# Optimization experiments

Hardware: AMD Instinct MI355X
Metric: run time of the kernel (lower is better)

The kernel has to match this reference:

```python
import jax, jax.numpy as jnp
import numpy as np

D_MODEL = 1024
N_HEADS = 16
D_K = D_MODEL // N_HEADS
SCALE = float(np.sqrt(D_K))


def setup_inputs() -> dict:
    key = jax.random.key(0)
    ks = jax.random.split(key, 9)
    B, L, D = 2, 2048, D_MODEL
    # xavier_uniform with gain 1/sqrt(2): limit = gain*sqrt(6/(fan_in+fan_out))
    limit = (1.0 / np.sqrt(2.0)) * np.sqrt(6.0 / (D + D))
    def xav(k):
        return jax.random.uniform(k, (D, D), jnp.float32, -limit, limit)
    return {
        "query": jax.random.normal(ks[0], (B, L, D), jnp.float32),
        "key": jax.random.normal(ks[1], (B, L, D), jnp.float32),
        "value": jax.random.normal(ks[2], (B, L, D), jnp.float32),
        "mask": jax.random.randint(ks[3], (B, L), 0, 2, jnp.int32),
        "w_q": xav(ks[4]),
        "w_k": xav(ks[5]),
        "w_v": xav(ks[6]),
        "w_o": xav(ks[7]),
        "b_o": jnp.zeros((D,), jnp.float32),
    }


def reference(query, key, value, mask, w_q, w_k, w_v, w_o, b_o):
    B, L, D = query.shape
    H, dk = N_HEADS, D_K
    # torch Linear: x @ W.T ; reshape to (B, H, L, dk)
    def proj(x, w):
        return (x @ w.T).reshape(B, L, H, dk).transpose(0, 2, 1, 3)
    Q = proj(query, w_q)
    K = proj(key, w_k)
    V = proj(value, w_v)
    scores = jnp.einsum("bhqd,bhkd->bhqk", Q, K) / SCALE
    scores = scores.astype(jnp.float32)
    keep = (mask != 0)[:, None, None, :]  # (B,1,1,L)
    scores = jnp.where(keep, scores, jnp.float32(-10000.0))
    attn = jax.nn.softmax(scores, axis=-1).astype(Q.dtype)
    # dropout is identity in eval mode
    ctx = jnp.einsum("bhqk,bhkd->bhqd", attn, V)
    ctx = ctx.transpose(0, 2, 1, 3).reshape(B, L, D)
    return ctx @ w_o.T + b_o
```

## Files before the change

kernel.cpp:

```cpp
#include <hip/hip_runtime.h>

#define DMODEL 1024
#define NHEADS 16
#define BATCH  2
#define SEQ    2048
#define MROWS  (BATCH * SEQ)

typedef unsigned short u16;
typedef unsigned int   u32;
typedef __attribute__((ext_vector_type(8))) short short8v;
typedef __attribute__((ext_vector_type(4))) short short4v;
typedef __attribute__((ext_vector_type(4))) int   int4v;
typedef __attribute__((ext_vector_type(4))) float f32x4;

#define SCALE_LOG2E 0.18033688011112042f

__device__ inline float bf2f(u16 u) {
  union { u32 i; float f; } c; c.i = ((u32)u) << 16; return c.f;
}
__device__ inline u16 f2bf(float f) {
  union { float f; u32 i; } c; c.f = f;
  u32 r = c.i + 0x7fffu + ((c.i >> 16) & 1u);
  return (u16)(r >> 16);
}
__device__ inline short8v ld8(const u16* p) { return *(const short8v*)p; }
__device__ inline short8v cvt8f(const float* p) {
  f32x4 v0 = *(const f32x4*)p;
  f32x4 v1 = *(const f32x4*)(p + 4);
  short8v r;
#pragma unroll
  for (int j = 0; j < 4; ++j) { r[j] = (short)f2bf(v0[j]); r[4 + j] = (short)f2bf(v1[j]); }
  return r;
}
__device__ inline void gload_lds16(const u16* g, u16* l) {
  __builtin_amdgcn_global_load_lds(
      (const __attribute__((address_space(1))) void*)g,
      (__attribute__((address_space(3))) void*)l, 16, 0, 0);
}
__device__ inline float exp2raw(float x) { return __builtin_amdgcn_exp2f(x); }
__device__ inline u32 pkbf(float a, float b) {
  u32 d; asm("v_cvt_pk_bf16_f32 %0, %1, %2" : "=v"(d) : "v"(a), "v"(b));
  return d;
}

__device__ inline int swz(int idx) {
  return idx ^ ((((idx >> 6) ^ (idx >> 9)) & 7) << 3);
}

__global__ __launch_bounds__(256) void cvt_all(
    const float* __restrict__ xq, const float* __restrict__ xk,
    const float* __restrict__ xv, const float* __restrict__ wq,
    const float* __restrict__ wk, const float* __restrict__ wv,
    const float* __restrict__ wo, u16* __restrict__ dst)
{
  int b = blockIdx.x;
  const float* s;
  u16* d;
  int local;
  if (b < 6144) {
    int which = b >> 11;
    s = (which == 0) ? xq : (which == 1) ? xk : xv;
    d = dst + (long)which * 4194304;
    local = b & 2047;
  } else {
    int wb = b - 6144;
    int which = wb >> 9;
    s = (which == 0) ? wq : (which == 1) ? wk : (which == 2) ? wv : wo;
    d = dst + 12582912 + (long)which * 1048576;
    local = wb & 511;
  }
  const long idx = ((long)local * 256 + threadIdx.x) * 8;
  *(short8v*)(d + idx) = cvt8f(s + idx);
}

__global__ __launch_bounds__(256) void gemm_bf(
    const u16* __restrict__ A0, const u16* __restrict__ A1, const u16* __restrict__ A2,
    const u16* __restrict__ W0, const u16* __restrict__ W1, const u16* __restrict__ W2,
    void* __restrict__ C0, void* __restrict__ C1, void* __restrict__ C2,
    const float* __restrict__ bias, int CF32, int Ndim, int Kdim)
{
  __shared__ __align__(16) u16 As[2][128 * 64];
  __shared__ __align__(16) u16 Bs[2][64 * 64];

  const int z = blockIdx.z;
  const u16* A = (z == 0) ? A0 : (z == 1) ? A1 : A2;
  const u16* W = (z == 0) ? W0 : (z == 1) ? W1 : W2;
  void* Craw   = (z == 0) ? C0 : (z == 1) ? C1 : C2;

  const int tid  = threadIdx.x;
  const int lane = tid & 63;
  const int w    = tid >> 6;
  const int wr   = w >> 1, wc = w & 1;
  const int r    = lane & 15, g = lane >> 4;

  const long brow = (long)blockIdx.x * 128;
  const long bcol = (long)blockIdx.y * 64;

  const int trow = tid >> 2;
  const int tk   = (tid & 3) * 8;

  const u16* Arow0 = A + (brow + trow) * (long)Kdim + tk;
  const u16* Arow1 = A + (brow + trow + 64) * (long)Kdim + tk;
  const u16* Wrow  = W + (bcol + trow) * (long)Kdim + tk;
  const int  woff  = w * 512;

  f32x4 acc[4][2] = {};

  gload_lds16(Arow0,      As[0] + woff);
  gload_lds16(Arow1,      As[0] + woff + 2048);
  gload_lds16(Arow0 + 32, As[0] + woff + 4096);
  gload_lds16(Arow1 + 32, As[0] + woff + 6144);
  gload_lds16(Wrow,       Bs[0] + woff);
  gload_lds16(Wrow + 32,  Bs[0] + woff + 2048);
  __syncthreads();

  int cur = 0;
  for (int k0 = 0; k0 < Kdim; k0 += 64) {
    if (k0 + 64 < Kdim) {
      const int kn = k0 + 64;
      gload_lds16(Arow0 + kn,      As[cur ^ 1] + woff);
      gload_lds16(Arow1 + kn,      As[cur ^ 1] + woff + 2048);
      gload_lds16(Arow0 + kn + 32, As[cur ^ 1] + woff + 4096);
      gload_lds16(Arow1 + kn + 32, As[cur ^ 1] + woff + 6144);
      gload_lds16(Wrow + kn,       Bs[cur ^ 1] + woff);
      gload_lds16(Wrow + kn + 32,  Bs[cur ^ 1] + woff + 2048);
    }

#pragma unroll
    for (int half = 0; half < 2; ++half) {
      const u16* Ah = As[cur] + half * 4096;
      const u16* Bh = Bs[cur] + half * 2048;
      short8v afr[4], bfr[2];
#pragma unroll
      for (int m = 0; m < 4; ++m)
        afr[m] = ld8(Ah + (wr * 64 + m * 16 + r) * 32 + g * 8);
#pragma unroll
      for (int n = 0; n < 2; ++n)
        bfr[n] = ld8(Bh + (wc * 32 + n * 16 + r) * 32 + g * 8);
#pragma unroll
      for (int m = 0; m < 4; ++m)
#pragma unroll
        for (int n = 0; n < 2; ++n)
          acc[m][n] = __builtin_amdgcn_mfma_f32_16x16x32_bf16(afr[m], bfr[n], acc[m][n], 0, 0, 0);
    }

    __syncthreads();
    cur ^= 1;
  }

#pragma unroll
  for (int n = 0; n < 2; ++n) {
    const long col = bcol + wc * 32 + n * 16 + r;
    const float bv = bias ? bias[col] : 0.0f;
#pragma unroll
    for (int m = 0; m < 4; ++m) {
#pragma unroll
      for (int r4 = 0; r4 < 4; ++r4) {
        const long row = brow + wr * 64 + m * 16 + g * 4 + r4;
        if (CF32) ((float*)Craw)[row * (long)Ndim + col] = acc[m][n][r4] + bv;
        else      ((u16*)Craw)[row * (long)Ndim + col]   = f2bf(acc[m][n][r4] + bv);
      }
    }
  }
}

__global__ __launch_bounds__(512) void attn_kernel(
    const u16* __restrict__ Q, const u16* __restrict__ K,
    const u16* __restrict__ V, const int* __restrict__ mask,
    u16* __restrict__ O)
{
  __shared__ __align__(16) u16 Ks[2][64 * 64];
  __shared__ __align__(16) u16 Vt[2][64 * 64];
  __shared__ __align__(16) u16 Ps[256 * 64];

  const int tid  = threadIdx.x;
  const int lane = tid & 63;
  const int w    = tid >> 6;
  const int r    = lane & 15, g = lane >> 4;

  const int slot = blockIdx.x;
  const int p    = (slot & 7) + 8 * (slot >> 6);
  const int x    = (slot >> 3) & 7;
  const int h    = p & 15;
  const int b    = p >> 4;

  const long wq = (long)b * SEQ + (long)x * 256 + w * 32;

  short8v qf[2][2];
#pragma unroll
  for (int qt = 0; qt < 2; ++qt)
#pragma unroll
    for (int ks = 0; ks < 2; ++ks)
      qf[qt][ks] = ld8(Q + (wq + qt * 16 + r) * DMODEL + h * 64 + ks * 32 + g * 8);

  f32x4 of[2][4] = {};
  float lsum[2] = {0.f, 0.f};

  const int trow = tid >> 3;
  const int td   = (tid & 7) * 8;

  const u16* Kb = K + (long)b * SEQ * DMODEL + h * 64;
  const u16* Vb = V + (long)b * SEQ * DMODEL + h * 64;
  const int* mb = mask + (long)b * SEQ;

  {
    short8v k0v = ld8(Kb + (long)trow * DMODEL + td);
    short8v v0v = ld8(Vb + (long)trow * DMODEL + td);
    *(short8v*)(Ks[0] + swz(trow * 64 + td)) = k0v;
#pragma unroll
    for (int j = 0; j < 8; ++j)
      Vt[0][swz((td + j) * 64 + trow)] = (u16)v0v[j];
  }

  int cur = 0;

  for (int t = 0; t < SEQ / 64; ++t) {
    const int kt0 = t * 64;
    const bool more = (t < SEQ / 64 - 1);

    int4v keepc[4];
#pragma unroll
    for (int kt = 0; kt < 4; ++kt)
      keepc[kt] = *(const int4v*)(mb + kt0 + kt * 16 + g * 4);

    short8v nk0, nv0;
    if (more) {
      nk0 = ld8(Kb + (long)(kt0 + 64 + trow) * DMODEL + td);
      nv0 = ld8(Vb + (long)(kt0 + 64 + trow) * DMODEL + td);
    }

    __syncthreads();

    const u16* Kc = Ks[cur];
    const u16* Vc = Vt[cur];

    f32x4 sf[2][4] = {};
#pragma unroll
    for (int ks = 0; ks < 2; ++ks) {
      short8v kf[4];
#pragma unroll
      for (int kt = 0; kt < 4; ++kt)
        kf[kt] = ld8(Kc + swz((kt * 16 + r) * 64 + ks * 32 + g * 8));
#pragma unroll
      for (int qt = 0; qt < 2; ++qt)
#pragma unroll
        for (int kt = 0; kt < 4; ++kt)
          sf[qt][kt] = __builtin_amdgcn_mfma_f32_16x16x32_bf16(kf[kt], qf[qt][ks], sf[qt][kt], 0, 0, 0);
    }

#pragma unroll
    for (int qt = 0; qt < 2; ++qt) {
      const int prow = (w * 32 + qt * 16 + r) * 64;
#pragma unroll
      for (int kt = 0; kt < 4; ++kt) {
        float p0 = keepc[kt][0] ? exp2raw(sf[qt][kt][0] * SCALE_LOG2E) : 0.f;
        float p1 = keepc[kt][1] ? exp2raw(sf[qt][kt][1] * SCALE_LOG2E) : 0.f;
        float p2 = keepc[kt][2] ? exp2raw(sf[qt][kt][2] * SCALE_LOG2E) : 0.f;
        float p3 = keepc[kt][3] ? exp2raw(sf[qt][kt][3] * SCALE_LOG2E) : 0.f;
        union { u32 u[2]; short4v s; } pk;
        pk.u[0] = pkbf(p0, p1);
        pk.u[1] = pkbf(p2, p3);
        *(short4v*)(Ps + swz(prow + kt * 16 + g * 4)) = pk.s;
        lsum[qt] += (p0 + p1) + (p2 + p3);
      }
    }

#pragma unroll
    for (int ks = 0; ks < 2; ++ks) {
      short8v vb[4];
#pragma unroll
      for (int dt = 0; dt < 4; ++dt)
        vb[dt] = ld8(Vc + swz((dt * 16 + r) * 64 + ks * 32 + g * 8));
#pragma unroll
      for (int qt = 0; qt < 2; ++qt) {
        short8v pa = ld8(Ps + swz((w * 32 + qt * 16 + r) * 64 + ks * 32 + g * 8));
#pragma unroll
        for (int dt = 0; dt < 4; ++dt)
          of[qt][dt] = __builtin_amdgcn_mfma_f32_16x16x32_bf16(pa, vb[dt], of[qt][dt], 0, 0, 0);
      }
    }

    if (more) {
      *(short8v*)(Ks[cur ^ 1] + swz(trow * 64 + td)) = nk0;
#pragma unroll
      for (int j = 0; j < 8; ++j)
        Vt[cur ^ 1][swz((td + j) * 64 + trow)] = (u16)nv0[j];
      cur ^= 1;
    }
  }

#pragma unroll
  for (int qt = 0; qt < 2; ++qt) {
    float s = lsum[qt];
    s += __shfl_xor(s, 16);
    s += __shfl_xor(s, 32);
#pragma unroll
    for (int r4 = 0; r4 < 4; ++r4) {
      const float d = __shfl(s, g * 4 + r4);
      const float rcp = (d > 0.f) ? (1.0f / d) : 0.0f;
#pragma unroll
      for (int dt = 0; dt < 4; ++dt) {
        const long row = wq + qt * 16 + g * 4 + r4;
        const int  col = h * 64 + dt * 16 + r;
        O[row * DMODEL + col] = f2bf(of[qt][dt][r4] * rcp);
      }
    }
  }
}

extern "C" void kernel_launch(void* const* d_in, const int* in_sizes, int n_in,
                              void* d_out, int out_size, void* d_ws, size_t ws_size,
                              hipStream_t stream) {
  const float* q_in = (const float*)d_in[0];
  const float* k_in = (const float*)d_in[1];
  const float* v_in = (const float*)d_in[2];
  const int*   mask = (const int*)d_in[3];
  const float* w_q  = (const float*)d_in[4];
  const float* w_k  = (const float*)d_in[5];
  const float* w_v  = (const float*)d_in[6];
  const float* w_o  = (const float*)d_in[7];
  const float* b_o  = (const float*)d_in[8];

  u16* S  = (u16*)d_ws;
  u16* Xq = S;
  u16* Xk = S + 4194304;
  u16* Xv = S + 8388608;
  u16* WQ = S + 12582912;
  u16* WK = S + 13631488;
  u16* WV = S + 14680064;
  u16* WO = S + 15728640;
  u16* Qw = (u16*)d_out;
  u16* Kw = Xq;
  u16* Vw = Xk;
  u16* Cw = Xv;

  dim3 blk(256);

  cvt_all<<<dim3(8192), blk, 0, stream>>>(q_in, k_in, v_in, w_q, w_k, w_v, w_o, S);

  dim3 pgrid(MROWS / 128, DMODEL / 64, 3);
  gemm_bf<<<pgrid, blk, 0, stream>>>(Xq, Xk, Xv, WQ, WK, WV,
                                     Qw, Kw, Vw, nullptr, 0, DMODEL, DMODEL);

  attn_kernel<<<dim3(256), dim3(512), 0, stream>>>(Qw, Kw, Vw, mask, Cw);

  dim3 ggrid(MROWS / 128, DMODEL / 64, 1);
  gemm_bf<<<ggrid, blk, 0, stream>>>(Cw, Cw, Cw, WO, WO, WO,
                                     (float*)d_out, (float*)d_out, (float*)d_out,
                                     b_o, 1, DMODEL, DMODEL);
}
```

Measured before the change: 127.1 us.

## Pre-transpose V in a separate kernel and stream K/V tiles via direct-to-LDS loads

Adds a kernel that writes V per head in pre-swizzled transposed 64x64 tiles into spare space in the output buffer. The attention kernel then fills its K and V shared-memory buffers with direct global-to-LDS loads (gload_lds16) instead of register staging and scalar transposed stores. The next tile's load is issued at the top of each iteration and a single barrier sits at the end. This removes the per-iteration scalar LDS transpose writes and register round trips, at the cost of an extra kernel launch and an extra read and write of V through global memory.

```diff
diff --git a/kernel.cpp b/kernel.cpp
--- a/kernel.cpp
+++ b/kernel.cpp
@@ -164,13 +164,33 @@
   }
 }
 
+__global__ __launch_bounds__(512) void transpose_v(
+    const u16* __restrict__ Vw, u16* __restrict__ VT)
+{
+  __shared__ __align__(16) u16 T[4096];
+
+  const int tid  = threadIdx.x;
+  const int tile = blockIdx.x, h = blockIdx.y, b = blockIdx.z;
+  const int trow = tid >> 3;
+  const int td   = (tid & 7) * 8;
+
+  short8v v = ld8(Vw + ((long)b * SEQ + tile * 64 + trow) * DMODEL + h * 64 + td);
+#pragma unroll
+  for (int j = 0; j < 8; ++j)
+    T[swz((td + j) * 64 + trow)] = (u16)v[j];
+  __syncthreads();
+
+  u16* dst = VT + (((long)(b * NHEADS + h) * 32 + tile) * 4096);
+  *(short8v*)(dst + tid * 8) = ld8(T + tid * 8);
+}
+
 __global__ __launch_bounds__(512) void attn_kernel(
     const u16* __restrict__ Q, const u16* __restrict__ K,
-    const u16* __restrict__ V, const int* __restrict__ mask,
+    const u16* __restrict__ VT, const int* __restrict__ mask,
     u16* __restrict__ O)
 {
-  __shared__ __align__(16) u16 Ks[2][64 * 64];
-  __shared__ __align__(16) u16 Vt[2][64 * 64];
+  __shared__ __align__(16) u16 Ks[2][4096];
+  __shared__ __align__(16) u16 Vt[2][4096];
   __shared__ __align__(16) u16 Ps[256 * 64];
 
   const int tid  = threadIdx.x;
@@ -196,40 +216,32 @@
   f32x4 of[2][4] = {};
   float lsum[2] = {0.f, 0.f};
 
-  const int trow = tid >> 3;
-  const int td   = (tid & 7) * 8;
-
-  const u16* Kb = K + (long)b * SEQ * DMODEL + h * 64;
-  const u16* Vb = V + (long)b * SEQ * DMODEL + h * 64;
+  const int u0   = swz(tid * 8);
+  const int key0 = u0 >> 6, dd0 = u0 & 63;
+  const u16* Ksrc = K + ((long)b * SEQ + key0) * DMODEL + h * 64 + dd0;
+  const u16* Vsrc = VT + ((long)(b * NHEADS + h) * 32) * 4096 + tid * 8;
+  const int  woff = w * 512;
+
   const int* mb = mask + (long)b * SEQ;
 
-  {
-    short8v k0v = ld8(Kb + (long)trow * DMODEL + td);
-    short8v v0v = ld8(Vb + (long)trow * DMODEL + td);
-    *(short8v*)(Ks[0] + swz(trow * 64 + td)) = k0v;
-#pragma unroll
-    for (int j = 0; j < 8; ++j)
-      Vt[0][swz((td + j) * 64 + trow)] = (u16)v0v[j];
-  }
+  gload_lds16(Ksrc, Ks[0] + woff);
+  gload_lds16(Vsrc, Vt[0] + woff);
+  __syncthreads();
 
   int cur = 0;
 
   for (int t = 0; t < SEQ / 64; ++t) {
     const int kt0 = t * 64;
-    const bool more = (t < SEQ / 64 - 1);
+
+    if (t + 1 < SEQ / 64) {
+      gload_lds16(Ksrc + (long)(t + 1) * 64 * DMODEL, Ks[cur ^ 1] + woff);
+      gload_lds16(Vsrc + (long)(t + 1) * 4096,        Vt[cur ^ 1] + woff);
+    }
 
     int4v keepc[4];
 #pragma unroll
     for (int kt = 0; kt < 4; ++kt)
       keepc[kt] = *(const int4v*)(mb + kt0 + kt * 16 + g * 4);
-
-    short8v nk0, nv0;
-    if (more) {
-      nk0 = ld8(Kb + (long)(kt0 + 64 + trow) * DMODEL + td);
-      nv0 = ld8(Vb + (long)(kt0 + 64 + trow) * DMODEL + td);
-    }
-
-    __syncthreads();
 
     const u16* Kc = Ks[cur];
     const u16* Vc = Vt[cur];
@@ -280,13 +292,8 @@
       }
     }
 
-    if (more) {
-      *(short8v*)(Ks[cur ^ 1] + swz(trow * 64 + td)) = nk0;
-#pragma unroll
-      for (int j = 0; j < 8; ++j)
-        Vt[cur ^ 1][swz((td + j) * 64 + trow)] = (u16)nv0[j];
-      cur ^= 1;
-    }
+    __syncthreads();
+    cur ^= 1;
   }
 
 #pragma unroll
@@ -330,6 +337,7 @@
   u16* WV = S + 14680064;
   u16* WO = S + 15728640;
   u16* Qw = (u16*)d_out;
+  u16* VTb = (u16*)d_out + 4194304;
   u16* Kw = Xq;
   u16* Vw = Xk;
   u16* Cw = Xv;
@@ -342,7 +350,10 @@
   gemm_bf<<<pgrid, blk, 0, stream>>>(Xq, Xk, Xv, WQ, WK, WV,
                                      Qw, Kw, Vw, nullptr, 0, DMODEL, DMODEL);
 
-  attn_kernel<<<dim3(256), dim3(512), 0, stream>>>(Qw, Kw, Vw, mask, Cw);
+  dim3 tgrid(SEQ / 64, NHEADS, BATCH);
+  transpose_v<<<tgrid, dim3(512), 0, stream>>>(Vw, VTb);
+
+  attn_kernel<<<dim3(256), dim3(512), 0, stream>>>(Qw, Kw, VTb, mask, Cw);
 
   dim3 ggrid(MROWS / 128, DMODEL / 64, 1);
   gemm_bf<<<ggrid, blk, 0, stream>>>(Cw, Cw, Cw, WO, WO, WO,
```

New measurement: 139.9 us. 10.1% more time.
